# Optimization experiments

Measured on AMD Instinct MI355X. Metric: run time of the kernel, lower is better.

Reference implementation:

```python
import jax, jax.numpy as jnp
import numpy as np

N = 4096   # nodes
E = 65536  # edges
D_IN = 64
H = 128
T = 8
B = 8


def setup_inputs() -> dict:
    key = jax.random.key(0)
    ks = jax.random.split(key, 6)
    x = jax.random.normal(ks[0], (B, T, N, D_IN), jnp.float32)
    edge_index = jax.random.randint(ks[1], (2, E), 0, N, dtype=jnp.int32)
    W0 = jax.random.normal(ks[2], (D_IN + H, 4 * H), jnp.float32) * 0.05
    b0 = jax.random.normal(ks[3], (4 * H,), jnp.float32) * 0.05
    W1 = jax.random.normal(ks[4], (H + H, 4 * H), jnp.float32) * 0.05
    b1 = jax.random.normal(ks[5], (4 * H,), jnp.float32) * 0.05
    return {"x": x, "W0": W0, "b0": b0, "W1": W1, "b1": b1, "edge_index": edge_index}


def _gcn_norm(edge_index, n):
    # PyG GCNConv(improved=True): A_hat = A + 2I, deg over incoming edges (col)
    src, dst = edge_index[0], edge_index[1]
    deg = jax.ops.segment_sum(jnp.ones(edge_index.shape[1], jnp.float32), dst, num_segments=n) + 2.0
    dinv = jax.lax.rsqrt(deg)  # deg >= 2 always, safe
    return src, dst, dinv


def _gcn_gates(comb, W, b, src, dst, dinv, n):
    # comb: (b, n, i+h) -> gates: (b, n, 4h)
    xw = jnp.einsum('bnf,fg->bng', comb, W)
    norm_e = dinv[src] * dinv[dst]                      # (E,)
    msgs = xw[:, src, :] * norm_e[None, :, None]        # (b, E, 4h)
    agg = jax.vmap(lambda m: jax.ops.segment_sum(m, dst, num_segments=n))(msgs)
    # self-loop with weight 2: norm = 2 * dinv[i]^2
    agg = agg + (2.0 * dinv * dinv)[None, :, None] * xw + b
    return agg


def reference(x, W0, b0, W1, b1, edge_index):
    src, dst, dinv = _gcn_norm(edge_index, N)

    def run_layer(seq, W, b):
        h_dim = W.shape[1] // 4

        def step(carry, xt):
            h, c = carry
            comb = jnp.concatenate([xt, h], axis=-1)
            gates = _gcn_gates(comb, W, b, src, dst, dinv, N)
            ci, cf, co, cg = jnp.split(gates, 4, axis=-1)
            i = jax.nn.sigmoid(ci)
            f = jax.nn.sigmoid(cf)
            o = jax.nn.sigmoid(co)
            g = jnp.tanh(cg)
            c_next = f * c + i * g
            h_next = o * jnp.tanh(c_next)
            return (h_next, c_next), h_next

        h0 = jnp.zeros((seq.shape[1], N, h_dim), seq.dtype)
        _, hs = jax.lax.scan(step, (h0, h0), seq)
        return hs  # (t, b, n, h)

    seq = jnp.swapaxes(x, 0, 1)  # batch_first -> (t, b, n, d)
    hs0 = run_layer(seq, W0, b0)
    hs1 = run_layer(hs0, W1, b1)
    return jnp.swapaxes(hs1, 0, 1)  # (b, t, n, h) last-layer output sequence
```

## Files before the change

kernel.cpp:

```cpp
#include <hip/hip_runtime.h>
#include <hip/hip_fp16.h>
#include <math.h>

constexpr int N_NODES = 4096;
constexpr int N_EDGES = 65536;
constexpr int D_INF   = 64;
constexpr int H       = 128;
constexpr int T       = 8;
constexpr int B       = 8;
constexpr int M       = B * N_NODES;

typedef __attribute__((ext_vector_type(8))) short bf16x8;
typedef __attribute__((ext_vector_type(4))) float f32x4;
typedef __attribute__((ext_vector_type(8))) _Float16 f16x8;

__device__ inline unsigned short f2bf(float x) {
  unsigned int u = __float_as_uint(x);
  unsigned int r = (u + 0x7fffu + ((u >> 16) & 1u)) >> 16;
  return (unsigned short)r;
}
__device__ inline float bf2f(unsigned short b) {
  return __uint_as_float((unsigned int)b << 16);
}
__device__ __forceinline__ int swz(int s) { return s ^ (((s >> 7) & 7) << 3); }


__global__ void k_count(const int* __restrict__ dst, int* __restrict__ cnt) {
  int e = blockIdx.x * blockDim.x + threadIdx.x;
  if (e < N_EDGES) atomicAdd(&cnt[dst[e]], 1);
}

__global__ void k_dinv(const int* __restrict__ cnt, float* __restrict__ dinv) {
  int n = blockIdx.x * blockDim.x + threadIdx.x;
  if (n < N_NODES) dinv[n] = 1.0f / sqrtf((float)cnt[n] + 2.0f);
}

__global__ void k_scan(const int* __restrict__ cnt, int* __restrict__ rowptr) {
  __shared__ int sums[1024];
  int t = threadIdx.x;
  int v0 = cnt[4*t+0], v1 = cnt[4*t+1], v2 = cnt[4*t+2], v3 = cnt[4*t+3];
  int s0 = v0, s1 = s0 + v1, s2 = s1 + v2, s3 = s2 + v3;
  sums[t] = s3;
  __syncthreads();
  for (int off = 1; off < 1024; off <<= 1) {
    int x = (t >= off) ? sums[t - off] : 0;
    __syncthreads();
    sums[t] += x;
    __syncthreads();
  }
  int base = (t > 0) ? sums[t - 1] : 0;
  if (t == 0) rowptr[0] = 0;
  rowptr[4*t+1] = base + s0;
  rowptr[4*t+2] = base + s1;
  rowptr[4*t+3] = base + s2;
  rowptr[4*t+4] = base + s3;
}

__global__ void k_fill(const int* __restrict__ src, const int* __restrict__ dst,
                       const float* __restrict__ dinv, const int* __restrict__ rowptr,
                       int* __restrict__ fill, int2* __restrict__ eg) {
  int e = blockIdx.x * blockDim.x + threadIdx.x;
  if (e >= N_EDGES) return;
  int s = src[e], d = dst[e];
  int p = rowptr[d] + atomicAdd(&fill[d], 1);
  eg[p] = make_int2(s, __float_as_int(dinv[s] * dinv[d]));
}

__global__ void k_hist(const int* __restrict__ cnt, int* __restrict__ hist) {
  int n = blockIdx.x * blockDim.x + threadIdx.x;
  if (n < N_NODES) atomicAdd(&hist[min(cnt[n], 127)], 1);
}

__global__ void k_hscan(const int* __restrict__ hist, int* __restrict__ hbase) {
  __shared__ int sh[128];
  int t = threadIdx.x;
  sh[t] = hist[t];
  __syncthreads();
  for (int off = 1; off < 128; off <<= 1) {
    int x = (t >= off) ? sh[t - off] : 0;
    __syncthreads();
    sh[t] += x;
    __syncthreads();
  }
  hbase[t] = sh[t] - hist[t];
}

__global__ void k_place(const int* __restrict__ cnt, const int* __restrict__ hbase,
                        int* __restrict__ filld, int* __restrict__ sorted) {
  int n = blockIdx.x * blockDim.x + threadIdx.x;
  if (n >= N_NODES) return;
  int d = min(cnt[n], 127);
  sorted[hbase[d] + atomicAdd(&filld[d], 1)] = n;
}

__global__ void k_pack(const float* __restrict__ W, unsigned short* __restrict__ Bp,
                       int K) {
  int tid = blockIdx.x * 256 + threadIdx.x;
  if (tid >= K * 64) return;
  int lane = tid & 63;
  int ntg  = (tid >> 6) & 31;
  int kb   = tid >> 11;
  int gate = ntg & 3, fg = ntg >> 2;
  int corig = gate * 128 + fg * 16 + (lane & 15);
  int k0 = kb * 32 + (lane >> 4) * 8;
  long obase = ((long)(kb * 32 + ntg) * 64 + lane) * 8;
  long plane = (long)K * 512;
  #pragma unroll
  for (int j = 0; j < 8; ++j) {
    float v = W[(long)(k0 + j) * 512 + corig];
    unsigned short h = f2bf(v);
    Bp[obase + j]         = h;
    Bp[plane + obase + j] = f2bf(v - bf2f(h));
  }
}

__global__ __launch_bounds__(512, 4) void k_l0(
    const int* __restrict__ rowptr, const int2* __restrict__ eg,
    const float* __restrict__ dinv, const int* __restrict__ sorted,
    const float* __restrict__ X32,
    const unsigned short* __restrict__ AH0,
    const unsigned short* __restrict__ Bp, const float* __restrict__ bias,
    _Float16* __restrict__ hout, float* __restrict__ cbuf) {
  __shared__ __align__(16) unsigned short Atx[8 * 2 * 64 * 8];
  __shared__ int nodeLDS[64];
  int tid  = threadIdx.x;
  int lane = tid & 63;
  int w    = tid >> 6;
  int j    = blockIdx.x;
  int b    = j & 7;
  int jj   = j >> 3;
  int g    = lane >> 4, l = lane & 15;
  int c4   = l * 4;
  const float* Ax = X32 + (long)b * ((long)T * N_NODES * D_INF);
  int kbA32  = c4 >> 5;
  int subA32 = (l & 7) >> 1;
  int j0A32  = (l & 1) * 4;

  #pragma unroll
  for (int nd = 0; nd < 2; ++nd) {
    int r  = (w << 3) + (g << 1) + nd;
    int pairIdx = jj * 32 + (r >> 1);
    int n  = (r & 1) ? sorted[N_NODES - 1 - pairIdx] : sorted[pairIdx];
    if (l == 0) nodeLDS[r] = n;
    int rs = rowptr[n], re = rowptr[n + 1];
    float accA[4] = {0.f, 0.f, 0.f, 0.f};
    int e = rs;
    for (; e + 3 < re; e += 4) {
      int2 q0 = eg[e], q1 = eg[e + 1], q2 = eg[e + 2], q3 = eg[e + 3];
      float w0 = __int_as_float(q0.y), w1 = __int_as_float(q1.y);
      float w2 = __int_as_float(q2.y), w3 = __int_as_float(q3.y);
      f32x4 a0 = *(const f32x4*)(Ax + (long)q0.x * D_INF + c4);
      f32x4 a1 = *(const f32x4*)(Ax + (long)q1.x * D_INF + c4);
      f32x4 a2 = *(const f32x4*)(Ax + (long)q2.x * D_INF + c4);
      f32x4 a3 = *(const f32x4*)(Ax + (long)q3.x * D_INF + c4);
      #pragma unroll
      for (int q = 0; q < 4; ++q)
        accA[q] += w0 * a0[q] + w1 * a1[q] + w2 * a2[q] + w3 * a3[q];
    }
    for (; e < re; ++e) {
      int2 q0 = eg[e];
      float w0 = __int_as_float(q0.y);
      f32x4 a0 = *(const f32x4*)(Ax + (long)q0.x * D_INF + c4);
      #pragma unroll
      for (int q = 0; q < 4; ++q) accA[q] += w0 * a0[q];
    }
    float dn = dinv[n];
    float sw = 2.0f * dn * dn;
    {
      f32x4 a = *(const f32x4*)(Ax + (long)n * D_INF + c4);
      #pragma unroll
      for (int q = 0; q < 4; ++q) accA[q] += sw * a[q];
    }
    unsigned long long hv = 0ull, lv = 0ull;
    #pragma unroll
    for (int q = 0; q < 4; ++q) {
      unsigned short hs = f2bf(accA[q]);
      unsigned short ls = f2bf(accA[q] - bf2f(hs));
      hv |= (unsigned long long)hs << (16 * q);
      lv |= (unsigned long long)ls << (16 * q);
    }
    int mt = r >> 4;
    int lA = (r & 15) + 16 * subA32;
    *(unsigned long long*)(Atx + swz(((mt * 2 + kbA32) * 64 + lA) * 8 + j0A32)) = hv;
    *(unsigned long long*)(Atx + swz((((4 + mt) * 2 + kbA32) * 64 + lA) * 8 + j0A32)) = lv;
  }
  __syncthreads();

  int l15 = lane & 15, lq = lane >> 4;
  const unsigned short* bb  = Bp + (long)(w * 4) * 512 + lane * 8;
  const unsigned short* blp = bb + (long)192 * 512;

  f32x4 acc[4][4];
  #pragma unroll
  for (int mt = 0; mt < 4; ++mt)
    #pragma unroll
    for (int gt = 0; gt < 4; ++gt)
      acc[mt][gt] = (f32x4){0.f, 0.f, 0.f, 0.f};

  __builtin_amdgcn_s_setprio(1);
  #pragma unroll
  for (int kb = 0; kb < 6; ++kb) {
    bf16x8 AH_[4], AL_[4];
    if (kb < 2) {
      #pragma unroll
      for (int mt = 0; mt < 4; ++mt) {
        AH_[mt] = *(const bf16x8*)(Atx + swz(((mt * 2 + kb) * 64 + lane) * 8));
        AL_[mt] = *(const bf16x8*)(Atx + swz((((4 + mt) * 2 + kb) * 64 + lane) * 8));
      }
    } else {
      #pragma unroll
      for (int mt = 0; mt < 4; ++mt) {
        AH_[mt] = *(const bf16x8*)(AH0 + ((((long)j * 8 + mt) * 4 + (kb - 2)) * 64 + lane) * 8);
        AL_[mt] = *(const bf16x8*)(AH0 + ((((long)j * 8 + 4 + mt) * 4 + (kb - 2)) * 64 + lane) * 8);
      }
    }
    bf16x8 BH[4], BL[4];
    #pragma unroll
    for (int gt = 0; gt < 4; ++gt) {
      BH[gt] = *(const bf16x8*)(bb  + ((long)kb * 32 + gt) * 512);
      BL[gt] = *(const bf16x8*)(blp + ((long)kb * 32 + gt) * 512);
    }
    #pragma unroll
    for (int gt = 0; gt < 4; ++gt) {
      #pragma unroll
      for (int mt = 0; mt < 4; ++mt) {
        acc[mt][gt] = __builtin_amdgcn_mfma_f32_16x16x32_bf16(AH_[mt], BH[gt], acc[mt][gt], 0, 0, 0);
        acc[mt][gt] = __builtin_amdgcn_mfma_f32_16x16x32_bf16(AL_[mt], BH[gt], acc[mt][gt], 0, 0, 0);
        acc[mt][gt] = __builtin_amdgcn_mfma_f32_16x16x32_bf16(AH_[mt], BL[gt], acc[mt][gt], 0, 0, 0);
      }
    }
  }
  __builtin_amdgcn_s_setprio(0);

  int f = w * 16 + l15;
  float bi = bias[f], bff = bias[128 + f], bo = bias[256 + f], bg = bias[384 + f];
  #pragma unroll
  for (int mt = 0; mt < 4; ++mt) {
    #pragma unroll
    for (int r = 0; r < 4; ++r) {
      int rt = mt * 16 + lq * 4 + r;
      int n2 = nodeLDS[rt];
      float vi = 1.0f / (1.0f + __expf(-(acc[mt][0][r] + bi)));
      float vf = 1.0f / (1.0f + __expf(-(acc[mt][1][r] + bff)));
      float vo = 1.0f / (1.0f + __expf(-(acc[mt][2][r] + bo)));
      float vg = tanhf(acc[mt][3][r] + bg);
      long idx = ((long)b * N_NODES + n2) * H + f;
      float cn = vf * cbuf[idx] + vi * vg;
      float hn = vo * tanhf(cn);
      cbuf[idx] = cn;
      hout[idx] = (_Float16)hn;
    }
  }
}

__global__ __launch_bounds__(512, 4) void k_l1(
    const int* __restrict__ rowptr, const int2* __restrict__ eg,
    const float* __restrict__ dinv, const int* __restrict__ sorted,
    const _Float16* __restrict__ H0,
    const _Float16* __restrict__ H1r,
    const unsigned short* __restrict__ Bp, const float* __restrict__ bias,
    unsigned short* __restrict__ AH0,
    _Float16* __restrict__ h1out, float* __restrict__ cbuf,
    float* __restrict__ out2, int t) {
  constexpr int KB = 8;
  __shared__ __align__(16) unsigned short At[8 * KB * 64 * 8];
  __shared__ int nodeLDS[64];
  int tid  = threadIdx.x;
  int lane = tid & 63;
  int w    = tid >> 6;
  int j    = blockIdx.x;
  int b    = j & 7;
  int jj   = j >> 3;
  int g    = lane >> 4, l = lane & 15;
  int c8   = l * 8;
  const _Float16* A_p = H0  + (long)b * N_NODES * H;
  const _Float16* B_p = H1r + (long)b * N_NODES * H;
  int lane2f = 16 * (l & 3);
  int kbA16  = c8 >> 5;
  int kbB    = 4 + kbA16;

  #pragma unroll
  for (int nd = 0; nd < 2; ++nd) {
    int r  = (w << 3) + (g << 1) + nd;
    int pairIdx = jj * 32 + (r >> 1);
    int n  = (r & 1) ? sorted[N_NODES - 1 - pairIdx] : sorted[pairIdx];
    if (l == 0) nodeLDS[r] = n;
    int rs = rowptr[n], re = rowptr[n + 1];
    float accA[8] = {0.f,0.f,0.f,0.f,0.f,0.f,0.f,0.f};
    float accB[8] = {0.f,0.f,0.f,0.f,0.f,0.f,0.f,0.f};
    int e = rs;
    for (; e + 3 < re; e += 4) {
      int2 q0 = eg[e], q1 = eg[e + 1], q2 = eg[e + 2], q3 = eg[e + 3];
      float w0 = __int_as_float(q0.y), w1 = __int_as_float(q1.y);
      float w2 = __int_as_float(q2.y), w3 = __int_as_float(q3.y);
      f16x8 a0 = *(const f16x8*)(A_p + (long)q0.x * H + c8);
      f16x8 a1 = *(const f16x8*)(A_p + (long)q1.x * H + c8);
      f16x8 a2 = *(const f16x8*)(A_p + (long)q2.x * H + c8);
      f16x8 a3 = *(const f16x8*)(A_p + (long)q3.x * H + c8);
      #pragma unroll
      for (int q = 0; q < 8; ++q)
        accA[q] += w0 * (float)a0[q] + w1 * (float)a1[q]
                 + w2 * (float)a2[q] + w3 * (float)a3[q];
      f16x8 b0 = *(const f16x8*)(B_p + (long)q0.x * H + c8);
      f16x8 b1 = *(const f16x8*)(B_p + (long)q1.x * H + c8);
      f16x8 b2 = *(const f16x8*)(B_p + (long)q2.x * H + c8);
      f16x8 b3 = *(const f16x8*)(B_p + (long)q3.x * H + c8);
      #pragma unroll
      for (int q = 0; q < 8; ++q)
        accB[q] += w0 * (float)b0[q] + w1 * (float)b1[q]
                 + w2 * (float)b2[q] + w3 * (float)b3[q];
    }
    for (; e < re; ++e) {
      int2 q0 = eg[e];
      float w0 = __int_as_float(q0.y);
      f16x8 a0 = *(const f16x8*)(A_p + (long)q0.x * H + c8);
      #pragma unroll
      for (int q = 0; q < 8; ++q) accA[q] += w0 * (float)a0[q];
      f16x8 b0 = *(const f16x8*)(B_p + (long)q0.x * H + c8);
      #pragma unroll
      for (int q = 0; q < 8; ++q) accB[q] += w0 * (float)b0[q];
    }
    float dn = dinv[n];
    float sw = 2.0f * dn * dn;
    {
      f16x8 a = *(const f16x8*)(A_p + (long)n * H + c8);
      f16x8 v = *(const f16x8*)(B_p + (long)n * H + c8);
      #pragma unroll
      for (int q = 0; q < 8; ++q) {
        accA[q] += sw * (float)a[q];
        accB[q] += sw * (float)v[q];
      }
    }

    int mt    = r >> 4;
    int lane2 = (r & 15) + lane2f;
    {
      bf16x8 hv, lv;
      #pragma unroll
      for (int q = 0; q < 8; ++q) {
        unsigned short hs = f2bf(accB[q]);
        hv[q] = (short)hs;
        lv[q] = (short)f2bf(accB[q] - bf2f(hs));
      }
      *(bf16x8*)(At + swz((((mt)     * KB + kbB) * 64 + lane2) * 8)) = hv;
      *(bf16x8*)(At + swz((((4 + mt) * KB + kbB) * 64 + lane2) * 8)) = lv;
    }
    {
      bf16x8 hv, lv;
      #pragma unroll
      for (int q = 0; q < 8; ++q) {
        unsigned short hs = f2bf(accA[q]);
        hv[q] = (short)hs;
        lv[q] = (short)f2bf(accA[q] - bf2f(hs));
      }
      *(bf16x8*)(At + swz((((mt)     * KB + kbA16) * 64 + lane2) * 8)) = hv;
      *(bf16x8*)(At + swz((((4 + mt) * KB + kbA16) * 64 + lane2) * 8)) = lv;
      *(bf16x8*)(AH0 + ((((long)j * 8 + mt)     * 4 + kbA16) * 64 + lane2) * 8) = hv;
      *(bf16x8*)(AH0 + ((((long)j * 8 + 4 + mt) * 4 + kbA16) * 64 + lane2) * 8) = lv;
    }
  }
  __syncthreads();

  int l15 = lane & 15, lq = lane >> 4;
  const unsigned short* bb  = Bp + (long)(w * 4) * 512 + lane * 8;
  const unsigned short* blp = bb + (long)256 * 512;

  f32x4 acc[4][4];
  #pragma unroll
  for (int mt = 0; mt < 4; ++mt)
    #pragma unroll
    for (int gt = 0; gt < 4; ++gt)
      acc[mt][gt] = (f32x4){0.f, 0.f, 0.f, 0.f};

  __builtin_amdgcn_s_setprio(1);
  #pragma unroll 2
  for (int kb = 0; kb < KB; ++kb) {
    bf16x8 AH_[4], AL_[4];
    #pragma unroll
    for (int mt = 0; mt < 4; ++mt) {
      AH_[mt] = *(const bf16x8*)(At + swz((((mt)     * KB + kb) * 64 + lane) * 8));
      AL_[mt] = *(const bf16x8*)(At + swz((((4 + mt) * KB + kb) * 64 + lane) * 8));
    }
    bf16x8 BH[4], BL[4];
    #pragma unroll
    for (int gt = 0; gt < 4; ++gt) {
      BH[gt] = *(const bf16x8*)(bb  + ((long)kb * 32 + gt) * 512);
      BL[gt] = *(const bf16x8*)(blp + ((long)kb * 32 + gt) * 512);
    }
    #pragma unroll
    for (int gt = 0; gt < 4; ++gt) {
      #pragma unroll
      for (int mt = 0; mt < 4; ++mt) {
        acc[mt][gt] = __builtin_amdgcn_mfma_f32_16x16x32_bf16(AH_[mt], BH[gt], acc[mt][gt], 0, 0, 0);
        acc[mt][gt] = __builtin_amdgcn_mfma_f32_16x16x32_bf16(AL_[mt], BH[gt], acc[mt][gt], 0, 0, 0);
        acc[mt][gt] = __builtin_amdgcn_mfma_f32_16x16x32_bf16(AH_[mt], BL[gt], acc[mt][gt], 0, 0, 0);
      }
    }
  }
  __builtin_amdgcn_s_setprio(0);

  int f = w * 16 + l15;
  float bi = bias[f], bff = bias[128 + f], bo = bias[256 + f], bg = bias[384 + f];
  #pragma unroll
  for (int mt = 0; mt < 4; ++mt) {
    #pragma unroll
    for (int r = 0; r < 4; ++r) {
      int rt = mt * 16 + lq * 4 + r;
      int n2 = nodeLDS[rt];
      float vi = 1.0f / (1.0f + __expf(-(acc[mt][0][r] + bi)));
      float vf = 1.0f / (1.0f + __expf(-(acc[mt][1][r] + bff)));
      float vo = 1.0f / (1.0f + __expf(-(acc[mt][2][r] + bo)));
      float vg = tanhf(acc[mt][3][r] + bg);
      long idx = ((long)b * N_NODES + n2) * H + f;
      float cn = vf * cbuf[idx] + vi * vg;
      float hn = vo * tanhf(cn);
      cbuf[idx] = cn;
      h1out[idx] = (_Float16)hn;
      __builtin_nontemporal_store(hn,
          &out2[(((long)b * T + t) * N_NODES + n2) * H + f]);
    }
  }
}


extern "C" void kernel_launch(void* const* d_in, const int* in_sizes, int n_in,
                              void* d_out, int out_size, void* d_ws, size_t ws_size,
                              hipStream_t stream) {
  const float* x  = (const float*)d_in[0];
  const float* W0 = (const float*)d_in[1];
  const float* b0 = (const float*)d_in[2];
  const float* W1 = (const float*)d_in[3];
  const float* b1 = (const float*)d_in[4];
  const int*   ei = (const int*)d_in[5];
  const int* srcp = ei;
  const int* dstp = ei + N_EDGES;
  float* out = (float*)d_out;

  char* p = (char*)d_ws;
  auto alloc = [&](size_t bytes) {
    char* r = p;
    p += (bytes + 255) & ~(size_t)255;
    return r;
  };
  int*   cnt    = (int*)  alloc(N_NODES * 4);
  int*   fill   = (int*)  alloc(N_NODES * 4);
  float* dinv   = (float*)alloc(N_NODES * 4);
  int*   rowptr = (int*)  alloc((N_NODES + 1) * 4);
  int2*  eg     = (int2*) alloc((size_t)N_EDGES * 8);
  int*   hist   = (int*)  alloc(128 * 4);
  int*   hbase  = (int*)  alloc(128 * 4);
  int*   filld  = (int*)  alloc(128 * 4);
  int*   sorted = (int*)  alloc(N_NODES * 4);
  float* cc     = (float*)alloc((size_t)2 * M * H * 4);
  _Float16* hh  = (_Float16*)alloc((size_t)3 * M * H * 2);
  unsigned short* AH0 = (unsigned short*)alloc((size_t)512 * 8 * 4 * 64 * 8 * 2);
  unsigned short* Bp0 = (unsigned short*)alloc((size_t)192 * 512 * 2 * 2);
  unsigned short* Bp1 = (unsigned short*)alloc((size_t)256 * 512 * 2 * 2);
  float*    c0  = cc;
  float*    c1  = cc + (size_t)M * H;
  _Float16* h0  = hh;
  _Float16* h1a = hh + (size_t)M * H;
  _Float16* h1b = hh + (size_t)2 * M * H;

  hipMemsetAsync(cnt,   0, N_NODES * 4, stream);
  hipMemsetAsync(fill,  0, N_NODES * 4, stream);
  hipMemsetAsync(hist,  0, 128 * 4, stream);
  hipMemsetAsync(filld, 0, 128 * 4, stream);
  hipMemsetAsync(cc,    0, (size_t)2 * M * H * 4, stream);
  hipMemsetAsync(hh,    0, (size_t)3 * M * H * 2, stream);
  hipMemsetAsync(AH0,   0, (size_t)512 * 8 * 4 * 64 * 8 * 2, stream);

  k_count<<<N_EDGES / 256, 256, 0, stream>>>(dstp, cnt);
  k_dinv <<<N_NODES / 256, 256, 0, stream>>>(cnt, dinv);
  k_scan <<<1, 1024, 0, stream>>>(cnt, rowptr);
  k_fill <<<N_EDGES / 256, 256, 0, stream>>>(srcp, dstp, dinv, rowptr, fill, eg);
  k_hist <<<N_NODES / 256, 256, 0, stream>>>(cnt, hist);
  k_hscan<<<1, 128, 0, stream>>>(hist, hbase);
  k_place<<<N_NODES / 256, 256, 0, stream>>>(cnt, hbase, filld, sorted);
  k_pack <<<(192 * 64 + 255) / 256, 256, 0, stream>>>(W0, Bp0, 192);
  k_pack <<<(256 * 64 + 255) / 256, 256, 0, stream>>>(W1, Bp1, 256);

  for (int t = 0; t < T; ++t) {
    const _Float16* h1r = (t & 1) ? h1b : h1a;
    _Float16*       h1w = (t & 1) ? h1a : h1b;
    k_l0<<<512, 512, 0, stream>>>(rowptr, eg, dinv, sorted,
        x + (size_t)t * N_NODES * D_INF, AH0, Bp0, b0, h0, c0);
    k_l1<<<512, 512, 0, stream>>>(rowptr, eg, dinv, sorted,
        h0, h1r, Bp1, b1, AH0, h1w, c1, out, t);
  }
}
```

Before: 806.7 us.

## Wavefront-pipeline layer0 step t+1 with layer1 step t in one launch

Merges the layer-0 and layer-1 kernels into one templated kernel and skews the schedule, so each launch runs layer 0 at step t+1 alongside layer 1 at step t using 1024 blocks. Launches drop from 16 to 9 and each one fills more of the GPU. Layer 0 now aggregates its own hidden-state neighbours in LDS instead of reading them from the AH0 buffer written by layer 1, so that buffer and its global stores go away. The cost is that layer 0 repeats the h gather work, and the hidden-state buffers are double-buffered.

```diff
diff --git a/kernel.cpp b/kernel.cpp
--- a/kernel.cpp
+++ b/kernel.cpp
@@ -114,24 +114,25 @@
   }
 }
 
-__global__ __launch_bounds__(512, 4) void k_l0(
+__device__ __forceinline__ void l0_body(
+    unsigned short* At, int* nodeLDS,
     const int* __restrict__ rowptr, const int2* __restrict__ eg,
     const float* __restrict__ dinv, const int* __restrict__ sorted,
-    const float* __restrict__ X32,
-    const unsigned short* __restrict__ AH0,
+    const float* __restrict__ X32, const _Float16* __restrict__ H0r,
     const unsigned short* __restrict__ Bp, const float* __restrict__ bias,
-    _Float16* __restrict__ hout, float* __restrict__ cbuf) {
-  __shared__ __align__(16) unsigned short Atx[8 * 2 * 64 * 8];
-  __shared__ int nodeLDS[64];
+    _Float16* __restrict__ h0w, float* __restrict__ cbuf, int jidx) {
+  constexpr int KB = 6;
   int tid  = threadIdx.x;
   int lane = tid & 63;
   int w    = tid >> 6;
-  int j    = blockIdx.x;
-  int b    = j & 7;
-  int jj   = j >> 3;
+  int b    = jidx & 7;
+  int jj   = jidx >> 3;
   int g    = lane >> 4, l = lane & 15;
-  int c4   = l * 4;
-  const float* Ax = X32 + (long)b * ((long)T * N_NODES * D_INF);
+  int c4   = l * 4, c8 = l * 8;
+  const float*    Ax = X32 + (long)b * ((long)T * N_NODES * D_INF);
+  const _Float16* Bh = H0r + (long)b * N_NODES * H;
+  int lane2f = 16 * (l & 3);
+  int kbB    = 2 + (c8 >> 5);
   int kbA32  = c4 >> 5;
   int subA32 = (l & 7) >> 1;
   int j0A32  = (l & 1) * 4;
@@ -143,7 +144,8 @@
     int n  = (r & 1) ? sorted[N_NODES - 1 - pairIdx] : sorted[pairIdx];
     if (l == 0) nodeLDS[r] = n;
     int rs = rowptr[n], re = rowptr[n + 1];
-    float accA[4] = {0.f, 0.f, 0.f, 0.f};
+    float accA[4] = {0.f,0.f,0.f,0.f};
+    float accB[8] = {0.f,0.f,0.f,0.f,0.f,0.f,0.f,0.f};
     int e = rs;
     for (; e + 3 < re; e += 4) {
       int2 q0 = eg[e], q1 = eg[e + 1], q2 = eg[e + 2], q3 = eg[e + 3];
@@ -156,6 +158,14 @@
       #pragma unroll
       for (int q = 0; q < 4; ++q)
         accA[q] += w0 * a0[q] + w1 * a1[q] + w2 * a2[q] + w3 * a3[q];
+      f16x8 b0 = *(const f16x8*)(Bh + (long)q0.x * H + c8);
+      f16x8 b1 = *(const f16x8*)(Bh + (long)q1.x * H + c8);
+      f16x8 b2 = *(const f16x8*)(Bh + (long)q2.x * H + c8);
+      f16x8 b3 = *(const f16x8*)(Bh + (long)q3.x * H + c8);
+      #pragma unroll
+      for (int q = 0; q < 8; ++q)
+        accB[q] += w0 * (float)b0[q] + w1 * (float)b1[q]
+                 + w2 * (float)b2[q] + w3 * (float)b3[q];
     }
     for (; e < re; ++e) {
       int2 q0 = eg[e];
@@ -163,26 +173,47 @@
       f32x4 a0 = *(const f32x4*)(Ax + (long)q0.x * D_INF + c4);
       #pragma unroll
       for (int q = 0; q < 4; ++q) accA[q] += w0 * a0[q];
+      f16x8 b0 = *(const f16x8*)(Bh + (long)q0.x * H + c8);
+      #pragma unroll
+      for (int q = 0; q < 8; ++q) accB[q] += w0 * (float)b0[q];
     }
     float dn = dinv[n];
     float sw = 2.0f * dn * dn;
     {
       f32x4 a = *(const f32x4*)(Ax + (long)n * D_INF + c4);
+      f16x8 v = *(const f16x8*)(Bh + (long)n * H + c8);
       #pragma unroll
       for (int q = 0; q < 4; ++q) accA[q] += sw * a[q];
-    }
-    unsigned long long hv = 0ull, lv = 0ull;
-    #pragma unroll
-    for (int q = 0; q < 4; ++q) {
-      unsigned short hs = f2bf(accA[q]);
-      unsigned short ls = f2bf(accA[q] - bf2f(hs));
-      hv |= (unsigned long long)hs << (16 * q);
-      lv |= (unsigned long long)ls << (16 * q);
-    }
-    int mt = r >> 4;
-    int lA = (r & 15) + 16 * subA32;
-    *(unsigned long long*)(Atx + swz(((mt * 2 + kbA32) * 64 + lA) * 8 + j0A32)) = hv;
-    *(unsigned long long*)(Atx + swz((((4 + mt) * 2 + kbA32) * 64 + lA) * 8 + j0A32)) = lv;
+      #pragma unroll
+      for (int q = 0; q < 8; ++q) accB[q] += sw * (float)v[q];
+    }
+
+    int mt    = r >> 4;
+    int lane2 = (r & 15) + lane2f;
+    {
+      bf16x8 hv, lv;
+      #pragma unroll
+      for (int q = 0; q < 8; ++q) {
+        unsigned short hs = f2bf(accB[q]);
+        hv[q] = (short)hs;
+        lv[q] = (short)f2bf(accB[q] - bf2f(hs));
+      }
+      *(bf16x8*)(At + swz((((mt)     * KB + kbB) * 64 + lane2) * 8)) = hv;
+      *(bf16x8*)(At + swz((((4 + mt) * KB + kbB) * 64 + lane2) * 8)) = lv;
+    }
+    {
+      unsigned long long hv = 0ull, lv = 0ull;
+      #pragma unroll
+      for (int q = 0; q < 4; ++q) {
+        unsigned short hs = f2bf(accA[q]);
+        unsigned short ls = f2bf(accA[q] - bf2f(hs));
+        hv |= (unsigned long long)hs << (16 * q);
+        lv |= (unsigned long long)ls << (16 * q);
+      }
+      int lA = (r & 15) + 16 * subA32;
+      *(unsigned long long*)(At + swz((((mt)     * KB + kbA32) * 64 + lA) * 8 + j0A32)) = hv;
+      *(unsigned long long*)(At + swz((((4 + mt) * KB + kbA32) * 64 + lA) * 8 + j0A32)) = lv;
+    }
   }
   __syncthreads();
 
@@ -198,21 +229,13 @@
       acc[mt][gt] = (f32x4){0.f, 0.f, 0.f, 0.f};
 
   __builtin_amdgcn_s_setprio(1);
-  #pragma unroll
-  for (int kb = 0; kb < 6; ++kb) {
+  #pragma unroll 2
+  for (int kb = 0; kb < KB; ++kb) {
     bf16x8 AH_[4], AL_[4];
-    if (kb < 2) {
-      #pragma unroll
-      for (int mt = 0; mt < 4; ++mt) {
-        AH_[mt] = *(const bf16x8*)(Atx + swz(((mt * 2 + kb) * 64 + lane) * 8));
-        AL_[mt] = *(const bf16x8*)(Atx + swz((((4 + mt) * 2 + kb) * 64 + lane) * 8));
-      }
-    } else {
-      #pragma unroll
-      for (int mt = 0; mt < 4; ++mt) {
-        AH_[mt] = *(const bf16x8*)(AH0 + ((((long)j * 8 + mt) * 4 + (kb - 2)) * 64 + lane) * 8);
-        AL_[mt] = *(const bf16x8*)(AH0 + ((((long)j * 8 + 4 + mt) * 4 + (kb - 2)) * 64 + lane) * 8);
-      }
+    #pragma unroll
+    for (int mt = 0; mt < 4; ++mt) {
+      AH_[mt] = *(const bf16x8*)(At + swz((((mt)     * KB + kb) * 64 + lane) * 8));
+      AL_[mt] = *(const bf16x8*)(At + swz((((4 + mt) * KB + kb) * 64 + lane) * 8));
     }
     bf16x8 BH[4], BL[4];
     #pragma unroll
@@ -248,29 +271,25 @@
       float cn = vf * cbuf[idx] + vi * vg;
       float hn = vo * tanhf(cn);
       cbuf[idx] = cn;
-      hout[idx] = (_Float16)hn;
-    }
-  }
-}
-
-__global__ __launch_bounds__(512, 4) void k_l1(
+      h0w[idx] = (_Float16)hn;
+    }
+  }
+}
+
+__device__ __forceinline__ void l1_body(
+    unsigned short* At, int* nodeLDS,
     const int* __restrict__ rowptr, const int2* __restrict__ eg,
     const float* __restrict__ dinv, const int* __restrict__ sorted,
-    const _Float16* __restrict__ H0,
-    const _Float16* __restrict__ H1r,
+    const _Float16* __restrict__ H0, const _Float16* __restrict__ H1r,
     const unsigned short* __restrict__ Bp, const float* __restrict__ bias,
-    unsigned short* __restrict__ AH0,
-    _Float16* __restrict__ h1out, float* __restrict__ cbuf,
-    float* __restrict__ out2, int t) {
+    _Float16* __restrict__ h1w, float* __restrict__ cbuf,
+    float* __restrict__ out2, int t, int jidx) {
   constexpr int KB = 8;
-  __shared__ __align__(16) unsigned short At[8 * KB * 64 * 8];
-  __shared__ int nodeLDS[64];
   int tid  = threadIdx.x;
   int lane = tid & 63;
   int w    = tid >> 6;
-  int j    = blockIdx.x;
-  int b    = j & 7;
-  int jj   = j >> 3;
+  int b    = jidx & 7;
+  int jj   = jidx >> 3;
   int g    = lane >> 4, l = lane & 15;
   int c8   = l * 8;
   const _Float16* A_p = H0  + (long)b * N_NODES * H;
@@ -355,8 +374,6 @@
       }
       *(bf16x8*)(At + swz((((mt)     * KB + kbA16) * 64 + lane2) * 8)) = hv;
       *(bf16x8*)(At + swz((((4 + mt) * KB + kbA16) * 64 + lane2) * 8)) = lv;
-      *(bf16x8*)(AH0 + ((((long)j * 8 + mt)     * 4 + kbA16) * 64 + lane2) * 8) = hv;
-      *(bf16x8*)(AH0 + ((((long)j * 8 + 4 + mt) * 4 + kbA16) * 64 + lane2) * 8) = lv;
     }
   }
   __syncthreads();
@@ -415,11 +432,43 @@
       float cn = vf * cbuf[idx] + vi * vg;
       float hn = vo * tanhf(cn);
       cbuf[idx] = cn;
-      h1out[idx] = (_Float16)hn;
+      h1w[idx] = (_Float16)hn;
       __builtin_nontemporal_store(hn,
           &out2[(((long)b * T + t) * N_NODES + n2) * H + f]);
     }
   }
+}
+
+template<int MODE>
+__global__ __launch_bounds__(512, 4) void k_step(
+    const int* __restrict__ rowptr, const int2* __restrict__ eg,
+    const float* __restrict__ dinv, const int* __restrict__ sorted,
+    const float* __restrict__ Xt1,
+    const _Float16* __restrict__ h0read,
+    _Float16* __restrict__ h0write,
+    const _Float16* __restrict__ h1read,
+    _Float16* __restrict__ h1write,
+    const unsigned short* __restrict__ Bp0, const float* __restrict__ b0,
+    const unsigned short* __restrict__ Bp1, const float* __restrict__ b1,
+    float* __restrict__ c0, float* __restrict__ c1,
+    float* __restrict__ out2, int t) {
+  __shared__ __align__(16) unsigned short At[8 * 8 * 64 * 8];
+  __shared__ int nodeLDS[64];
+  int j = blockIdx.x;
+  int role, jidx;
+  if constexpr (MODE == 2) {
+    role = (j >> 3) & 1;
+    jidx = ((j >> 4) << 3) | (j & 7);
+  } else {
+    role = (MODE == 0) ? 0 : 1;
+    jidx = j;
+  }
+  if (role == 0)
+    l1_body(At, nodeLDS, rowptr, eg, dinv, sorted, h0read, h1read,
+            Bp1, b1, h1write, c1, out2, t, jidx);
+  else
+    l0_body(At, nodeLDS, rowptr, eg, dinv, sorted, Xt1, h0read,
+            Bp0, b0, h0write, c0, jidx);
 }
 
 
@@ -452,23 +501,22 @@
   int*   filld  = (int*)  alloc(128 * 4);
   int*   sorted = (int*)  alloc(N_NODES * 4);
   float* cc     = (float*)alloc((size_t)2 * M * H * 4);
-  _Float16* hh  = (_Float16*)alloc((size_t)3 * M * H * 2);
-  unsigned short* AH0 = (unsigned short*)alloc((size_t)512 * 8 * 4 * 64 * 8 * 2);
+  _Float16* hh  = (_Float16*)alloc((size_t)4 * M * H * 2);
   unsigned short* Bp0 = (unsigned short*)alloc((size_t)192 * 512 * 2 * 2);
   unsigned short* Bp1 = (unsigned short*)alloc((size_t)256 * 512 * 2 * 2);
   float*    c0  = cc;
   float*    c1  = cc + (size_t)M * H;
-  _Float16* h0  = hh;
-  _Float16* h1a = hh + (size_t)M * H;
-  _Float16* h1b = hh + (size_t)2 * M * H;
+  _Float16* h0a = hh;
+  _Float16* h0b = hh + (size_t)M * H;
+  _Float16* h1a = hh + (size_t)2 * M * H;
+  _Float16* h1b = hh + (size_t)3 * M * H;
 
   hipMemsetAsync(cnt,   0, N_NODES * 4, stream);
   hipMemsetAsync(fill,  0, N_NODES * 4, stream);
   hipMemsetAsync(hist,  0, 128 * 4, stream);
   hipMemsetAsync(filld, 0, 128 * 4, stream);
   hipMemsetAsync(cc,    0, (size_t)2 * M * H * 4, stream);
-  hipMemsetAsync(hh,    0, (size_t)3 * M * H * 2, stream);
-  hipMemsetAsync(AH0,   0, (size_t)512 * 8 * 4 * 64 * 8 * 2, stream);
+  hipMemsetAsync(hh,    0, (size_t)4 * M * H * 2, stream);
 
   k_count<<<N_EDGES / 256, 256, 0, stream>>>(dstp, cnt);
   k_dinv <<<N_NODES / 256, 256, 0, stream>>>(cnt, dinv);
@@ -480,12 +528,21 @@
   k_pack <<<(192 * 64 + 255) / 256, 256, 0, stream>>>(W0, Bp0, 192);
   k_pack <<<(256 * 64 + 255) / 256, 256, 0, stream>>>(W1, Bp1, 256);
 
-  for (int t = 0; t < T; ++t) {
-    const _Float16* h1r = (t & 1) ? h1b : h1a;
-    _Float16*       h1w = (t & 1) ? h1a : h1b;
-    k_l0<<<512, 512, 0, stream>>>(rowptr, eg, dinv, sorted,
-        x + (size_t)t * N_NODES * D_INF, AH0, Bp0, b0, h0, c0);
-    k_l1<<<512, 512, 0, stream>>>(rowptr, eg, dinv, sorted,
-        h0, h1r, Bp1, b1, AH0, h1w, c1, out, t);
-  }
-}
+  auto h0buf = [&](int tt) { return (tt & 1) ? h0b : h0a; };
+  auto h1buf = [&](int tt) { return (tt & 1) ? h1b : h1a; };
+
+  k_step<1><<<512, 512, 0, stream>>>(rowptr, eg, dinv, sorted,
+      x, h0buf(-1), h0buf(0), nullptr, nullptr,
+      Bp0, b0, Bp1, b1, c0, c1, nullptr, 0);
+
+  for (int t = 0; t < T - 1; ++t) {
+    k_step<2><<<1024, 512, 0, stream>>>(rowptr, eg, dinv, sorted,
+        x + (size_t)(t + 1) * N_NODES * D_INF,
+        h0buf(t), h0buf(t + 1), h1buf(t - 1), h1buf(t),
+        Bp0, b0, Bp1, b1, c0, c1, out, t);
+  }
+
+  k_step<0><<<512, 512, 0, stream>>>(rowptr, eg, dinv, sorted,
+      nullptr, h0buf(T - 1), nullptr, h1buf(T - 2), h1buf(T - 1),
+      Bp0, b0, Bp1, b1, c0, c1, out, T - 1);
+}
```

Result: faster. 733.4 us (-9.1%).
